# Optimization experiments

Measured on AMD Instinct MI355X. Metric: run time of the kernel, lower is better.

The kernel has to match this reference:

```python
import jax, jax.numpy as jnp
import numpy as np

B, N, CS = 4, 384, 384
CZ = 128
H, C, PQ, PV = 12, 16, 4, 8
INF, EPS = 1e5, 1e-8


def _rigid_apply(rot, trans, pts):
    # rot: [B,N,3,3], trans: [B,N,3], pts: [B,N,P,3]
    return jnp.einsum('bnij,bnpj->bnpi', rot, pts) + trans[:, :, None, :]


def _pts_from_linear(x, n_pts):
    # torch: split last dim into 3 chunks (x,y,z blocks) then stack on dim -1
    Bx, Nx = x.shape[:2]
    return jnp.moveaxis(x.reshape(Bx, Nx, 3, n_pts), -2, -1)  # [B,N,n_pts,3]


def _forward(s, z, rot, trans, mask, w_q, b_q, w_kv, b_kv, w_gq, b_gq, w_gk, b_gk,
             w_qp, b_qp, w_kvp, b_kvp, head_weights, w_out, b_out):
    del z  # z is an unused arg in the original forward
    Bx, Nx, _ = s.shape
    q = (s @ w_q + b_q).reshape(Bx, Nx, H, C)
    kv = (s @ w_kv + b_kv).reshape(Bx, Nx, H, 2 * C)
    k, v = kv[..., :C], kv[..., C:]
    # g_q / g_k are computed in the original but never used (dead code):
    _ = (s.sum(0) @ w_gq + b_gq)
    _ = (s.sum(0) @ w_gk + b_gk)

    q_pts = _pts_from_linear(s @ w_qp + b_qp, H * PQ)
    q_pts = _rigid_apply(rot, trans, q_pts).reshape(Bx, Nx, H, PQ, 3)
    kv_pts = _pts_from_linear(s @ w_kvp + b_kvp, H * (PQ + PV))
    kv_pts = _rigid_apply(rot, trans, kv_pts).reshape(Bx, Nx, H, PQ + PV, 3)
    k_pts, v_pts = kv_pts[..., :PQ, :], kv_pts[..., PQ:, :]

    scale = np.sqrt(1.0 / (3 * C)).astype(np.float32)
    a = jnp.einsum('bihc,bjhc->bhij', q, k) * scale  # [B,H,N,N]
    a_g = a  # original recomputes the identical q@k product

    # point-distance attention bias; diff is [B,N,N,H,PQ,3]
    diff = q_pts[:, :, None] - k_pts[:, None]
    sq = jnp.sum(diff * diff, axis=-1)  # [B,N,N,H,PQ]
    hw = jax.nn.softplus(head_weights) * np.sqrt(1.0 / (3 * (PQ * 9.0 / 2))).astype(np.float32)
    pt_att = -0.5 * jnp.sum(sq * hw[:, None], axis=-1)  # [B,N,N,H]
    pt_att = jnp.moveaxis(pt_att, -1, 1)  # [B,H,N,N]

    square_mask = INF * (mask[:, :, None] * mask[:, None, :] - 1.0)  # [B,N,N]
    a = jax.nn.softmax(a + square_mask[:, None] + a_g + pt_att, axis=-1)

    o = jnp.einsum('bhij,bjhc->bihc', a, v).reshape(Bx, Nx, H * C)
    o_pt = jnp.einsum('bhij,bjhpx->bihpx', a, v_pts)  # [B,N,H,PV,3]
    # invert_apply: rot^T (x - t)
    o_pt = jnp.einsum('bnji,bnhpj->bnhpi', rot, o_pt - trans[:, :, None, None, :])
    o_pt_norm = jnp.sqrt(jnp.sum(o_pt ** 2, axis=-1) + EPS).reshape(Bx, Nx, H * PV)
    o_pt = o_pt.reshape(Bx, Nx, H * PV, 3)
    cat = jnp.concatenate([o, o_pt[..., 0], o_pt[..., 1], o_pt[..., 2], o_pt_norm], axis=-1)
    return cat @ w_out + b_out


def setup_inputs() -> dict:
    key = jax.random.key(0)
    ks = jax.random.split(key, 16)
    lin = lambda k, fi, fo: jax.random.normal(k, (fi, fo), jnp.float32) / np.sqrt(fi).astype(np.float32)
    hc = H * C
    out_dim = H * (C + PV * 4)
    return {
        's': jax.random.normal(ks[0], (B, N, CS), jnp.float32),
        'z': jax.random.normal(ks[1], (B, N, N, CZ), jnp.float32),
        'rot': jnp.linalg.qr(jax.random.normal(ks[2], (B, N, 3, 3), jnp.float32))[0],
        'trans': jax.random.normal(ks[3], (B, N, 3), jnp.float32),
        'mask': jnp.ones((B, N), jnp.float32),
        'w_q': lin(ks[4], CS, hc), 'b_q': jnp.zeros((hc,), jnp.float32),
        'w_kv': lin(ks[5], CS, 2 * hc), 'b_kv': jnp.zeros((2 * hc,), jnp.float32),
        'w_gq': lin(ks[6], CS, hc), 'b_gq': jnp.zeros((hc,), jnp.float32),
        'w_gk': lin(ks[7], CS, hc), 'b_gk': jnp.zeros((hc,), jnp.float32),
        'w_qp': lin(ks[8], CS, H * PQ * 3), 'b_qp': jnp.zeros((H * PQ * 3,), jnp.float32),
        'w_kvp': lin(ks[9], CS, H * (PQ + PV) * 3), 'b_kvp': jnp.zeros((H * (PQ + PV) * 3,), jnp.float32),
        'head_weights': jnp.full((H,), 0.541324854, jnp.float32),  # softplus^-1(1)
        'w_out': lin(ks[10], out_dim, CS), 'b_out': jnp.zeros((CS,), jnp.float32),
    }


def reference(s, z, rot, trans, mask, w_q, b_q, w_kv, b_kv, w_gq, b_gq, w_gk, b_gk,
              w_qp, b_qp, w_kvp, b_kvp, head_weights, w_out, b_out):
    return _forward(s, z, rot, trans, mask, w_q, b_q, w_kv, b_kv, w_gq, b_gq, w_gk, b_gk,
                    w_qp, b_qp, w_kvp, b_kvp, head_weights, w_out, b_out)
```

## Files before the change

kernel.cpp:

```cpp
#include <hip/hip_runtime.h>
#include <math.h>

#define Bb 4
#define Nn 384
#define CSs 384
#define Hh 12
#define Cc 16
#define PQq 4
#define PVv 8
#define FPROJ 1152
#define FCAT 576
#define INFV 100000.0f
#define EPSV 1e-8f

#define WS_PROJ 0
#define WS_KP   1769472
#define WS_VP   2064384
#define WS_KPP  2359296
#define WS_VPP  2580480
#define WS_CAT  3022848
#define WS_QP   3907584
#define WS_QPP  4202496
#define WS_PART 4423680
#define PSTRIDE 2688
#define WS_WT   9068544
#define WS_WTO  9289728

typedef __attribute__((ext_vector_type(8))) short short8v;
typedef __attribute__((ext_vector_type(4))) float f32x4;

__device__ __forceinline__ short f2bf(float x) {
    unsigned u = __float_as_uint(x);
    unsigned r = (u + 0x7FFFu + ((u >> 16) & 1u)) >> 16;
    return (short)r;
}

__device__ __forceinline__ float get_bias(int f,
    const float* __restrict__ b_q, const float* __restrict__ b_kv,
    const float* __restrict__ b_qp, const float* __restrict__ b_kvp)
{
    if (f < 192) return b_q[f];
    if (f < 576) return b_kv[f - 192];
    if (f < 720) return b_qp[f - 576];
    return b_kvp[f - 720];
}

__global__ __launch_bounds__(256) void prep_kernel(
    const float* __restrict__ w_q, const float* __restrict__ w_kv,
    const float* __restrict__ w_qp, const float* __restrict__ w_kvp,
    const float* __restrict__ w_out,
    short* __restrict__ wt, short* __restrict__ wto)
{
    int idx = blockIdx.x * 256 + threadIdx.x;
    if (idx < 1152 * 384) {
        int f = idx / 384, k = idx % 384;
        float v;
        if (f < 192)      v = w_q[(size_t)k * 192 + f];
        else if (f < 576) v = w_kv[(size_t)k * 384 + (f - 192)];
        else if (f < 720) v = w_qp[(size_t)k * 144 + (f - 576)];
        else              v = w_kvp[(size_t)k * 432 + (f - 720)];
        wt[idx] = f2bf(v);
    } else if (idx < 1152 * 384 + 384 * 576) {
        int j = idx - 1152 * 384;
        int f = j / 576, k = j % 576;
        wto[j] = f2bf(w_out[(size_t)k * 384 + f]);
    }
}

__global__ __launch_bounds__(256) void proj_kernel(
    const float* __restrict__ s, const short* __restrict__ wt,
    const float* __restrict__ b_q, const float* __restrict__ b_kv,
    const float* __restrict__ b_qp, const float* __restrict__ b_kvp,
    float* __restrict__ proj)
{
    __shared__ short Al[64 * 40];
    __shared__ short Bl[64 * 40];

    const int bm = blockIdx.x % 24;
    const int bn = blockIdx.x / 24;
    const int m0 = bm * 64;
    const int f0 = bn * 64;
    const int t = threadIdx.x;
    const int w = t >> 6;
    const int lane = t & 63;
    const int lrow = lane & 15;
    const int lkg  = lane >> 4;

    const int srow = t >> 2;
    const int sseg = t & 3;

    f32x4 acc0 = {0,0,0,0}, acc1 = {0,0,0,0}, acc2 = {0,0,0,0}, acc3 = {0,0,0,0};

    for (int ks = 0; ks < 12; ++ks) {
        const int kbase = ks * 32;
        {
            const float* sp = s + (size_t)(m0 + srow) * CSs + kbase + sseg * 8;
            float4 v0 = *(const float4*)sp;
            float4 v1 = *(const float4*)(sp + 4);
            short8v a;
            a[0]=f2bf(v0.x); a[1]=f2bf(v0.y); a[2]=f2bf(v0.z); a[3]=f2bf(v0.w);
            a[4]=f2bf(v1.x); a[5]=f2bf(v1.y); a[6]=f2bf(v1.z); a[7]=f2bf(v1.w);
            *(short8v*)&Al[srow * 40 + sseg * 8] = a;
        }
        {
            short8v bvv = *(const short8v*)&wt[(size_t)(f0 + srow) * 384 + kbase + sseg * 8];
            *(short8v*)&Bl[srow * 40 + sseg * 8] = bvv;
        }
        __syncthreads();

        short8v av = *(const short8v*)&Al[(16 * w + lrow) * 40 + lkg * 8];
        short8v b0 = *(const short8v*)&Bl[(lrow) * 40 + lkg * 8];
        short8v b1 = *(const short8v*)&Bl[(16 + lrow) * 40 + lkg * 8];
        short8v b2 = *(const short8v*)&Bl[(32 + lrow) * 40 + lkg * 8];
        short8v b3 = *(const short8v*)&Bl[(48 + lrow) * 40 + lkg * 8];
        acc0 = __builtin_amdgcn_mfma_f32_16x16x32_bf16(av, b0, acc0, 0, 0, 0);
        acc1 = __builtin_amdgcn_mfma_f32_16x16x32_bf16(av, b1, acc1, 0, 0, 0);
        acc2 = __builtin_amdgcn_mfma_f32_16x16x32_bf16(av, b2, acc2, 0, 0, 0);
        acc3 = __builtin_amdgcn_mfma_f32_16x16x32_bf16(av, b3, acc3, 0, 0, 0);
        __syncthreads();
    }

    const int orow = m0 + 16 * w + lkg * 4;
#pragma unroll
    for (int e = 0; e < 4; ++e) {
        float* pr = proj + (size_t)(orow + e) * FPROJ + f0;
        int c0 = lrow;
        pr[c0]      = acc0[e] + get_bias(f0 + c0,      b_q, b_kv, b_qp, b_kvp);
        pr[16 + c0] = acc1[e] + get_bias(f0 + 16 + c0, b_q, b_kv, b_qp, b_kvp);
        pr[32 + c0] = acc2[e] + get_bias(f0 + 32 + c0, b_q, b_kv, b_qp, b_kvp);
        pr[48 + c0] = acc3[e] + get_bias(f0 + 48 + c0, b_q, b_kv, b_qp, b_kvp);
    }
}

__global__ __launch_bounds__(192) void pack_kernel(
    const float* __restrict__ proj,
    const float* __restrict__ rot, const float* __restrict__ trans,
    const float* __restrict__ hwts,
    float* __restrict__ Kp, float* __restrict__ Vp,
    float* __restrict__ KPp, float* __restrict__ VPp,
    float* __restrict__ Qp, float* __restrict__ QPp)
{
    const int bn = blockIdx.x;
    const int b = bn / Nn;
    const int n = bn % Nn;
    const int t = threadIdx.x;
    const float* R = rot + (size_t)bn * 9;
    const float* T = trans + (size_t)bn * 3;
    const float* pr = proj + (size_t)bn * FPROJ;

    if (t < 144) {
        float x = pr[720 + t];
        float y = pr[720 + 144 + t];
        float z = pr[720 + 288 + t];
        float ox = R[0]*x + R[1]*y + R[2]*z + T[0];
        float oy = R[3]*x + R[4]*y + R[5]*z + T[1];
        float oz = R[6]*x + R[7]*y + R[8]*z + T[2];
        int h = t / 12, pp = t % 12;
        int bh = b * Hh + h;
        if (pp < PQq) {
            float* o = KPp + ((size_t)(bh * Nn + n)) * 12 + pp * 3;
            o[0] = ox; o[1] = oy; o[2] = oz;
        } else {
            float* o = VPp + ((size_t)(bh * Nn + n)) * 24 + (pp - PQq) * 3;
            o[0] = ox; o[1] = oy; o[2] = oz;
        }
    }
    if (t < 48) {
        float x = pr[576 + t];
        float y = pr[576 + 48 + t];
        float z = pr[576 + 96 + t];
        float ox = R[0]*x + R[1]*y + R[2]*z + T[0];
        float oy = R[3]*x + R[4]*y + R[5]*z + T[1];
        float oz = R[6]*x + R[7]*y + R[8]*z + T[2];
        int h = t / 4, p = t % 4;
        float hw2 = log1pf(expf(hwts[h]));
        float n2wc = hw2 * 0.13608276348795434f;
        float* o = QPp + ((size_t)((b * Hh + h) * Nn + n)) * 12 + p * 3;
        o[0] = n2wc * ox; o[1] = n2wc * oy; o[2] = n2wc * oz;
    }
#pragma unroll
    for (int rep = 0; rep < 2; ++rep) {
        int idx = t + rep * 192;
        {
            int h = idx / 32, c2 = idx % 32;
            int bh = b * Hh + h;
            float v = pr[192 + h * 32 + c2];
            if (c2 < 16) Kp[((size_t)(bh * Nn + n)) * 16 + c2] = v;
            else         Vp[((size_t)(bh * Nn + n)) * 16 + (c2 - 16)] = v;
        }
        if (idx < 192) {
            int h = idx >> 4, c = idx & 15;
            int bh = b * Hh + h;
            Qp[((size_t)(bh * Nn + n)) * 16 + c] = 0.28867513459481287f * pr[idx];
        }
    }
}

__device__ __forceinline__ void store_hilo(short* H, short* L, int off, const float* vals) {
    short8v h0, h1, l0, l1;
#pragma unroll
    for (int k = 0; k < 8; ++k) {
        short hh = f2bf(vals[k]);
        float hf = __uint_as_float(((unsigned)(unsigned short)hh) << 16);
        h0[k] = hh; l0[k] = f2bf(vals[k] - hf);
    }
#pragma unroll
    for (int k = 0; k < 8; ++k) {
        short hh = f2bf(vals[k + 8]);
        float hf = __uint_as_float(((unsigned)(unsigned short)hh) << 16);
        h1[k] = hh; l1[k] = f2bf(vals[k + 8] - hf);
    }
    *(short8v*)&H[off]     = h0; *(short8v*)&H[off + 8] = h1;
    *(short8v*)&L[off]     = l0; *(short8v*)&L[off + 8] = l1;
}

__global__ __launch_bounds__(256) void attn_part_kernel(
    const float* __restrict__ Qp, const float* __restrict__ QPp,
    const float* __restrict__ Kp, const float* __restrict__ Vp,
    const float* __restrict__ KPp, const float* __restrict__ VPp,
    const float* __restrict__ mask, const float* __restrict__ hwts,
    float* __restrict__ part)
{
    __shared__ short smem_s[13696];
    short* Ahi = smem_s;
    short* Alo = smem_s + 2560;
    short* Khi = smem_s + 5120;
    short* Klo = smem_s + 7680;
    short* Vb  = smem_s + 10240;
    short* Pb  = smem_s;

    const int bid = blockIdx.x;
    const int jc = bid % 6;
    const int ic = (bid / 6) % 6;
    const int h  = (bid / 36) % Hh;
    const int b  = bid / (36 * Hh);
    const int t  = threadIdx.x;
    const int i0 = ic * 64;
    const int j0 = jc * 64;
    const int bh = b * Hh + h;

    const float hw = log1pf(expf(hwts[h]));
    const float wc = -0.5f * hw * 0.13608276348795434f;

    const float* QpB  = Qp  + ((size_t)(bh * Nn + i0)) * 16;
    const float* QPpB = QPp + ((size_t)(bh * Nn + i0)) * 12;
    const float* KpB  = Kp  + ((size_t)(bh * Nn + j0)) * 16;
    const float* VpB  = Vp  + ((size_t)(bh * Nn + j0)) * 16;
    const float* KPpB = KPp + ((size_t)(bh * Nn + j0)) * 12;
    const float* VPpB = VPp + ((size_t)(bh * Nn + j0)) * 24;
    const float* mb   = mask + b * Nn;

    if (t < 128) {
        const int i = t >> 1, half = t & 1;
        float vals[16];
        if (half == 0) {
            float4 a0 = *(const float4*)(QpB + i * 16);
            float4 a1 = *(const float4*)(QpB + i * 16 + 4);
            float4 a2 = *(const float4*)(QpB + i * 16 + 8);
            float4 a3 = *(const float4*)(QpB + i * 16 + 12);
            vals[0]=a0.x; vals[1]=a0.y; vals[2]=a0.z; vals[3]=a0.w;
            vals[4]=a1.x; vals[5]=a1.y; vals[6]=a1.z; vals[7]=a1.w;
            vals[8]=a2.x; vals[9]=a2.y; vals[10]=a2.z; vals[11]=a2.w;
            vals[12]=a3.x; vals[13]=a3.y; vals[14]=a3.z; vals[15]=a3.w;
        } else {
            float4 a0 = *(const float4*)(QPpB + i * 12);
            float4 a1 = *(const float4*)(QPpB + i * 12 + 4);
            float4 a2 = *(const float4*)(QPpB + i * 12 + 8);
            vals[0]=a0.x; vals[1]=a0.y; vals[2]=a0.z; vals[3]=a0.w;
            vals[4]=a1.x; vals[5]=a1.y; vals[6]=a1.z; vals[7]=a1.w;
            vals[8]=a2.x; vals[9]=a2.y; vals[10]=a2.z; vals[11]=a2.w;
            vals[12] = 1.0f;
            vals[13] = mb[i0 + i];
            vals[14] = 0.0f; vals[15] = 0.0f;
        }
        store_hilo(Ahi, Alo, i * 40 + half * 16, vals);
    } else {
        const int tt = t - 128, j = tt >> 1, half = tt & 1;
        float vals[16];
        if (half == 0) {
            float4 a0 = *(const float4*)(KpB + j * 16);
            float4 a1 = *(const float4*)(KpB + j * 16 + 4);
            float4 a2 = *(const float4*)(KpB + j * 16 + 8);
            float4 a3 = *(const float4*)(KpB + j * 16 + 12);
            vals[0]=a0.x; vals[1]=a0.y; vals[2]=a0.z; vals[3]=a0.w;
            vals[4]=a1.x; vals[5]=a1.y; vals[6]=a1.z; vals[7]=a1.w;
            vals[8]=a2.x; vals[9]=a2.y; vals[10]=a2.z; vals[11]=a2.w;
            vals[12]=a3.x; vals[13]=a3.y; vals[14]=a3.z; vals[15]=a3.w;
        } else {
            float4 a0 = *(const float4*)(KPpB + j * 12);
            float4 a1 = *(const float4*)(KPpB + j * 12 + 4);
            float4 a2 = *(const float4*)(KPpB + j * 12 + 8);
            vals[0]=a0.x; vals[1]=a0.y; vals[2]=a0.z; vals[3]=a0.w;
            vals[4]=a1.x; vals[5]=a1.y; vals[6]=a1.z; vals[7]=a1.w;
            vals[8]=a2.x; vals[9]=a2.y; vals[10]=a2.z; vals[11]=a2.w;
            float sq = a0.x*a0.x + a0.y*a0.y + a0.z*a0.z + a0.w*a0.w
                     + a1.x*a1.x + a1.y*a1.y + a1.z*a1.z + a1.w*a1.w
                     + a2.x*a2.x + a2.y*a2.y + a2.z*a2.z + a2.w*a2.w;
            vals[12] = wc * sq;
            vals[13] = INFV * (mb[j0 + j] - 1.0f);
            vals[14] = 0.0f; vals[15] = 0.0f;
        }
        store_hilo(Khi, Klo, j * 40 + half * 16, vals);
    }
    if (t < 128) {
        const int j = t >> 1, q = t & 1;
        float vv[20];
        if (q == 0) {
            float4 a0 = *(const float4*)(VpB + j * 16);
            float4 a1 = *(const float4*)(VpB + j * 16 + 4);
            float4 a2 = *(const float4*)(VpB + j * 16 + 8);
            float4 a3 = *(const float4*)(VpB + j * 16 + 12);
            float4 a4 = *(const float4*)(VPpB + j * 24);
            vv[0]=a0.x; vv[1]=a0.y; vv[2]=a0.z; vv[3]=a0.w;
            vv[4]=a1.x; vv[5]=a1.y; vv[6]=a1.z; vv[7]=a1.w;
            vv[8]=a2.x; vv[9]=a2.y; vv[10]=a2.z; vv[11]=a2.w;
            vv[12]=a3.x; vv[13]=a3.y; vv[14]=a3.z; vv[15]=a3.w;
            vv[16]=a4.x; vv[17]=a4.y; vv[18]=a4.z; vv[19]=a4.w;
        } else {
            float4 a0 = *(const float4*)(VPpB + j * 24 + 4);
            float4 a1 = *(const float4*)(VPpB + j * 24 + 8);
            float4 a2 = *(const float4*)(VPpB + j * 24 + 12);
            float4 a3 = *(const float4*)(VPpB + j * 24 + 16);
            float4 a4 = *(const float4*)(VPpB + j * 24 + 20);
            vv[0]=a0.x; vv[1]=a0.y; vv[2]=a0.z; vv[3]=a0.w;
            vv[4]=a1.x; vv[5]=a1.y; vv[6]=a1.z; vv[7]=a1.w;
            vv[8]=a2.x; vv[9]=a2.y; vv[10]=a2.z; vv[11]=a2.w;
            vv[12]=a3.x; vv[13]=a3.y; vv[14]=a3.z; vv[15]=a3.w;
            vv[16]=a4.x; vv[17]=a4.y; vv[18]=a4.z; vv[19]=a4.w;
        }
        const int c0 = q * 20;
#pragma unroll
        for (int k = 0; k < 20; ++k)
            Vb[(c0 + k) * 72 + j] = f2bf(vv[k]);
    } else {
        const int tt = t - 128;
        const int r = 40 + (tt >> 4);
        const int c0 = (tt & 15) * 4;
        Vb[r * 72 + c0 + 0] = 0; Vb[r * 72 + c0 + 1] = 0;
        Vb[r * 72 + c0 + 2] = 0; Vb[r * 72 + c0 + 3] = 0;
    }
    __syncthreads();

    const int w = t >> 6;
    const int lane = t & 63;
    const int lrow = lane & 15;
    const int lkg  = lane >> 4;

    f32x4 La0 = {0,0,0,0}, La1 = {0,0,0,0}, La2 = {0,0,0,0}, La3 = {0,0,0,0};
    {
        short8v ahi = *(const short8v*)&Ahi[(16 * w + lrow) * 40 + lkg * 8];
        short8v alo = *(const short8v*)&Alo[(16 * w + lrow) * 40 + lkg * 8];
        short8v k0h = *(const short8v*)&Khi[(lrow) * 40 + lkg * 8];
        short8v k1h = *(const short8v*)&Khi[(16 + lrow) * 40 + lkg * 8];
        short8v k2h = *(const short8v*)&Khi[(32 + lrow) * 40 + lkg * 8];
        short8v k3h = *(const short8v*)&Khi[(48 + lrow) * 40 + lkg * 8];
        short8v k0l = *(const short8v*)&Klo[(lrow) * 40 + lkg * 8];
        short8v k1l = *(const short8v*)&Klo[(16 + lrow) * 40 + lkg * 8];
        short8v k2l = *(const short8v*)&Klo[(32 + lrow) * 40 + lkg * 8];
        short8v k3l = *(const short8v*)&Klo[(48 + lrow) * 40 + lkg * 8];
        La0 = __builtin_amdgcn_mfma_f32_16x16x32_bf16(ahi, k0h, La0, 0, 0, 0);
        La1 = __builtin_amdgcn_mfma_f32_16x16x32_bf16(ahi, k1h, La1, 0, 0, 0);
        La2 = __builtin_amdgcn_mfma_f32_16x16x32_bf16(ahi, k2h, La2, 0, 0, 0);
        La3 = __builtin_amdgcn_mfma_f32_16x16x32_bf16(ahi, k3h, La3, 0, 0, 0);
        La0 = __builtin_amdgcn_mfma_f32_16x16x32_bf16(alo, k0h, La0, 0, 0, 0);
        La1 = __builtin_amdgcn_mfma_f32_16x16x32_bf16(alo, k1h, La1, 0, 0, 0);
        La2 = __builtin_amdgcn_mfma_f32_16x16x32_bf16(alo, k2h, La2, 0, 0, 0);
        La3 = __builtin_amdgcn_mfma_f32_16x16x32_bf16(alo, k3h, La3, 0, 0, 0);
        La0 = __builtin_amdgcn_mfma_f32_16x16x32_bf16(ahi, k0l, La0, 0, 0, 0);
        La1 = __builtin_amdgcn_mfma_f32_16x16x32_bf16(ahi, k1l, La1, 0, 0, 0);
        La2 = __builtin_amdgcn_mfma_f32_16x16x32_bf16(ahi, k2l, La2, 0, 0, 0);
        La3 = __builtin_amdgcn_mfma_f32_16x16x32_bf16(ahi, k3l, La3, 0, 0, 0);
    }

    const size_t pidx = ((size_t)(bh * 6 + ic)) * 6 + jc;
    float* po = part + pidx * PSTRIDE;

    float m0_, m1_, m2_, m3_, s0_, s1_, s2_, s3_;
    float p00,p10,p20,p30, p01,p11,p21,p31, p02,p12,p22,p32, p03,p13,p23,p33;

#define SMAX_E(E, TM, SM, P0, P1, P2, P3) { \
    float tmax_ = fmaxf(fmaxf(La0[E], La1[E]), fmaxf(La2[E], La3[E])); \
    tmax_ = fmaxf(tmax_, __shfl_xor(tmax_, 1)); \
    tmax_ = fmaxf(tmax_, __shfl_xor(tmax_, 2)); \
    tmax_ = fmaxf(tmax_, __shfl_xor(tmax_, 4)); \
    tmax_ = fmaxf(tmax_, __shfl_xor(tmax_, 8)); \
    P0 = __expf(La0[E] - tmax_); P1 = __expf(La1[E] - tmax_); \
    P2 = __expf(La2[E] - tmax_); P3 = __expf(La3[E] - tmax_); \
    float cs_ = P0 + P1 + P2 + P3; \
    cs_ += __shfl_xor(cs_, 1); cs_ += __shfl_xor(cs_, 2); \
    cs_ += __shfl_xor(cs_, 4); cs_ += __shfl_xor(cs_, 8); \
    TM = tmax_; SM = cs_; }

    SMAX_E(0, m0_, s0_, p00, p10, p20, p30);
    SMAX_E(1, m1_, s1_, p01, p11, p21, p31);
    SMAX_E(2, m2_, s2_, p02, p12, p22, p32);
    SMAX_E(3, m3_, s3_, p03, p13, p23, p33);
#undef SMAX_E

    if (lrow == 0) {
        int rb = 16 * w + 4 * lkg;
        po[2560 + rb + 0] = m0_; po[2624 + rb + 0] = s0_;
        po[2560 + rb + 1] = m1_; po[2624 + rb + 1] = s1_;
        po[2560 + rb + 2] = m2_; po[2624 + rb + 2] = s2_;
        po[2560 + rb + 3] = m3_; po[2624 + rb + 3] = s3_;
    }
    __syncthreads();

#define PW(E, PJ0, PJ1, PJ2, PJ3) { \
    int r_ = (16 * w + 4 * lkg + E) * 72; \
    Pb[r_ + lrow]      = f2bf(PJ0); \
    Pb[r_ + 16 + lrow] = f2bf(PJ1); \
    Pb[r_ + 32 + lrow] = f2bf(PJ2); \
    Pb[r_ + 48 + lrow] = f2bf(PJ3); }
    PW(0, p00, p10, p20, p30);
    PW(1, p01, p11, p21, p31);
    PW(2, p02, p12, p22, p32);
    PW(3, p03, p13, p23, p33);
#undef PW
    __syncthreads();

    f32x4 O0 = {0,0,0,0}, O1 = {0,0,0,0}, O2 = {0,0,0,0};
#pragma unroll
    for (int ch = 0; ch < 2; ++ch) {
        short8v pf = *(const short8v*)&Pb[(16 * w + lrow) * 72 + ch * 32 + lkg * 8];
        short8v v0 = *(const short8v*)&Vb[(lrow) * 72 + ch * 32 + lkg * 8];
        short8v v1 = *(const short8v*)&Vb[(16 + lrow) * 72 + ch * 32 + lkg * 8];
        short8v v2 = *(const short8v*)&Vb[(32 + lrow) * 72 + ch * 32 + lkg * 8];
        O0 = __builtin_amdgcn_mfma_f32_16x16x32_bf16(pf, v0, O0, 0, 0, 0);
        O1 = __builtin_amdgcn_mfma_f32_16x16x32_bf16(pf, v1, O1, 0, 0, 0);
        O2 = __builtin_amdgcn_mfma_f32_16x16x32_bf16(pf, v2, O2, 0, 0, 0);
    }
#pragma unroll
    for (int e = 0; e < 4; ++e) {
        int r = 16 * w + 4 * lkg + e;
        po[r * 40 + lrow]      = O0[e];
        po[r * 40 + 16 + lrow] = O1[e];
        if (lrow < 8) po[r * 40 + 32 + lrow] = O2[e];
    }
}

__global__ __launch_bounds__(256) void attn_merge_kernel(
    const float* __restrict__ part,
    const float* __restrict__ rot, const float* __restrict__ trans,
    float* __restrict__ cat)
{
    __shared__ float wsh[64 * 8];
    __shared__ float ob[64 * 44];

    const int bid = blockIdx.x;
    const int ic = bid % 6;
    const int h  = (bid / 6) % Hh;
    const int b  = bid / (6 * Hh);
    const int t  = threadIdx.x;
    const int i0 = ic * 64;
    const int bh = b * Hh + h;
    const size_t pbase = (((size_t)(bh * 6 + ic)) * 6) * PSTRIDE;

    if (t < 64) {
        float mk[6], sk[6];
        float M = -3.0e38f;
#pragma unroll
        for (int k = 0; k < 6; ++k) {
            mk[k] = part[pbase + (size_t)k * PSTRIDE + 2560 + t];
            sk[k] = part[pbase + (size_t)k * PSTRIDE + 2624 + t];
            M = fmaxf(M, mk[k]);
        }
        float wk[6]; float stot = 0.0f;
#pragma unroll
        for (int k = 0; k < 6; ++k) {
            wk[k] = __expf(mk[k] - M);
            stot += wk[k] * sk[k];
        }
        float inv = 1.0f / stot;
#pragma unroll
        for (int k = 0; k < 6; ++k) wsh[t * 8 + k] = wk[k] * inv;
    }
    __syncthreads();

#pragma unroll
    for (int it = 0; it < 10; ++it) {
        int idx = t + it * 256;
        int row = idx / 40, col = idx % 40;
        float v = 0.0f;
#pragma unroll
        for (int k = 0; k < 6; ++k)
            v += wsh[row * 8 + k] * part[pbase + (size_t)k * PSTRIDE + row * 40 + col];
        ob[row * 44 + col] = v;
    }
    __syncthreads();

    {
        const int i = t >> 2;
        const int qq = t & 3;
        const int bnI = b * Nn + i0 + i;
        float* crow = cat + (size_t)bnI * FCAT;

        float4 o = *(const float4*)&ob[i * 44 + 4 * qq];
        *(float4*)&crow[h * 16 + 4 * qq] = o;

        const float* R = rot + (size_t)bnI * 9;
        const float* T = trans + (size_t)bnI * 3;
#pragma unroll
        for (int e = 0; e < 2; ++e) {
            int pe = qq + 4 * e;
            float g0 = ob[i * 44 + 16 + 3 * pe + 0] - T[0];
            float g1 = ob[i * 44 + 16 + 3 * pe + 1] - T[1];
            float g2 = ob[i * 44 + 16 + 3 * pe + 2] - T[2];
            float lx = R[0]*g0 + R[3]*g1 + R[6]*g2;
            float ly = R[1]*g0 + R[4]*g1 + R[7]*g2;
            float lz = R[2]*g0 + R[5]*g1 + R[8]*g2;
            crow[192 + h * 8 + pe] = lx;
            crow[288 + h * 8 + pe] = ly;
            crow[384 + h * 8 + pe] = lz;
            crow[480 + h * 8 + pe] = sqrtf(lx*lx + ly*ly + lz*lz + EPSV);
        }
    }
}

__global__ __launch_bounds__(256) void out_kernel(
    const float* __restrict__ cat, const short* __restrict__ wto,
    const float* __restrict__ b_out, float* __restrict__ out)
{
    __shared__ short Al[64 * 40];
    __shared__ short Bl[64 * 40];

    const int bm = blockIdx.x % 24;
    const int bn = blockIdx.x / 24;
    const int m0 = bm * 64;
    const int n0 = bn * 64;
    const int t = threadIdx.x;
    const int w = t >> 6;
    const int lane = t & 63;
    const int lrow = lane & 15;
    const int lkg  = lane >> 4;

    const int srow = t >> 2;
    const int sseg = t & 3;

    f32x4 acc0 = {0,0,0,0}, acc1 = {0,0,0,0}, acc2 = {0,0,0,0}, acc3 = {0,0,0,0};

    for (int ks = 0; ks < 18; ++ks) {
        const int kbase = ks * 32;
        {
            const float* cp = cat + (size_t)(m0 + srow) * FCAT + kbase + sseg * 8;
            float4 v0 = *(const float4*)cp;
            float4 v1 = *(const float4*)(cp + 4);
            short8v a;
            a[0]=f2bf(v0.x); a[1]=f2bf(v0.y); a[2]=f2bf(v0.z); a[3]=f2bf(v0.w);
            a[4]=f2bf(v1.x); a[5]=f2bf(v1.y); a[6]=f2bf(v1.z); a[7]=f2bf(v1.w);
            *(short8v*)&Al[srow * 40 + sseg * 8] = a;
        }
        {
            short8v bvv = *(const short8v*)&wto[(size_t)(n0 + srow) * FCAT + kbase + sseg * 8];
            *(short8v*)&Bl[srow * 40 + sseg * 8] = bvv;
        }
        __syncthreads();

        short8v av = *(const short8v*)&Al[(16 * w + lrow) * 40 + lkg * 8];
        short8v b0 = *(const short8v*)&Bl[(lrow) * 40 + lkg * 8];
        short8v b1 = *(const short8v*)&Bl[(16 + lrow) * 40 + lkg * 8];
        short8v b2 = *(const short8v*)&Bl[(32 + lrow) * 40 + lkg * 8];
        short8v b3 = *(const short8v*)&Bl[(48 + lrow) * 40 + lkg * 8];
        acc0 = __builtin_amdgcn_mfma_f32_16x16x32_bf16(av, b0, acc0, 0, 0, 0);
        acc1 = __builtin_amdgcn_mfma_f32_16x16x32_bf16(av, b1, acc1, 0, 0, 0);
        acc2 = __builtin_amdgcn_mfma_f32_16x16x32_bf16(av, b2, acc2, 0, 0, 0);
        acc3 = __builtin_amdgcn_mfma_f32_16x16x32_bf16(av, b3, acc3, 0, 0, 0);
        __syncthreads();
    }

    const int orow = m0 + 16 * w + lkg * 4;
#pragma unroll
    for (int e = 0; e < 4; ++e) {
        float* pr = out + (size_t)(orow + e) * 384 + n0;
        int c0 = lrow;
        pr[c0]      = acc0[e] + b_out[n0 + c0];
        pr[16 + c0] = acc1[e] + b_out[n0 + 16 + c0];
        pr[32 + c0] = acc2[e] + b_out[n0 + 32 + c0];
        pr[48 + c0] = acc3[e] + b_out[n0 + 48 + c0];
    }
}

extern "C" void kernel_launch(void* const* d_in, const int* in_sizes, int n_in,
                              void* d_out, int out_size, void* d_ws, size_t ws_size,
                              hipStream_t stream) {
    const float* s     = (const float*)d_in[0];
    const float* rot   = (const float*)d_in[2];
    const float* trans = (const float*)d_in[3];
    const float* mask  = (const float*)d_in[4];
    const float* w_q   = (const float*)d_in[5];
    const float* b_q   = (const float*)d_in[6];
    const float* w_kv  = (const float*)d_in[7];
    const float* b_kv  = (const float*)d_in[8];
    const float* w_qp  = (const float*)d_in[13];
    const float* b_qp  = (const float*)d_in[14];
    const float* w_kvp = (const float*)d_in[15];
    const float* b_kvp = (const float*)d_in[16];
    const float* hwts  = (const float*)d_in[17];
    const float* w_out = (const float*)d_in[18];
    const float* b_out = (const float*)d_in[19];

    float* ws    = (float*)d_ws;
    float* proj  = ws + WS_PROJ;
    float* Kp    = ws + WS_KP;
    float* Vp    = ws + WS_VP;
    float* KPp   = ws + WS_KPP;
    float* VPp   = ws + WS_VPP;
    float* catb  = ws + WS_CAT;
    float* Qp    = ws + WS_QP;
    float* QPp   = ws + WS_QPP;
    float* partb = ws + WS_PART;
    short* wt    = (short*)(ws + WS_WT);
    short* wto   = (short*)(ws + WS_WTO);
    float* out   = (float*)d_out;

    hipLaunchKernelGGL(prep_kernel, dim3(2592), dim3(256), 0, stream,
                       w_q, w_kv, w_qp, w_kvp, w_out, wt, wto);
    hipLaunchKernelGGL(proj_kernel, dim3(432), dim3(256), 0, stream,
                       s, wt, b_q, b_kv, b_qp, b_kvp, proj);
    hipLaunchKernelGGL(pack_kernel, dim3(1536), dim3(192), 0, stream,
                       proj, rot, trans, hwts, Kp, Vp, KPp, VPp, Qp, QPp);
    hipLaunchKernelGGL(attn_part_kernel, dim3(1728), dim3(256), 0, stream,
                       Qp, QPp, Kp, Vp, KPp, VPp, mask, hwts, partb);
    hipLaunchKernelGGL(attn_merge_kernel, dim3(288), dim3(256), 0, stream,
                       partb, rot, trans, catb);
    hipLaunchKernelGGL(out_kernel, dim3(144), dim3(256), 0, stream,
                       catb, wto, b_out, out);
}
```

Before: 60.20 us.

## Pre-pack bf16 hi/lo attention operands in pack kernel and store concat as bf16

The pack kernel now builds the augmented Q/K rows (scaled q, weighted points, mask and squared-norm columns) and the V rows, splits them into bf16 hi/lo pairs, and writes them in the layout the attention kernel stages into shared memory. The attention kernel then copies bf16 vectors instead of redoing the conversion and norm work in each of its 36 tiles per head. The merge kernel also writes the concatenated features as bf16, which halves the traffic read by the output GEMM. In exchange the pack kernel does more work and uses shared memory, and the workspace gains new buffers.

```diff
diff --git a/kernel.cpp b/kernel.cpp
--- a/kernel.cpp
+++ b/kernel.cpp
@@ -14,17 +14,16 @@
 #define EPSV 1e-8f
 
 #define WS_PROJ 0
-#define WS_KP   1769472
-#define WS_VP   2064384
-#define WS_KPP  2359296
-#define WS_VPP  2580480
 #define WS_CAT  3022848
-#define WS_QP   3907584
-#define WS_QPP  4202496
 #define WS_PART 4423680
 #define PSTRIDE 2688
 #define WS_WT   9068544
 #define WS_WTO  9289728
+#define WS_AH   9400320
+#define WS_AL   9695232
+#define WS_KH   9990144
+#define WS_KL   10285056
+#define WS_VBP  10579968
 
 typedef __attribute__((ext_vector_type(8))) short short8v;
 typedef __attribute__((ext_vector_type(4))) float f32x4;
@@ -33,6 +32,9 @@
     unsigned u = __float_as_uint(x);
     unsigned r = (u + 0x7FFFu + ((u >> 16) & 1u)) >> 16;
     return (short)r;
+}
+__device__ __forceinline__ float bf2f(short h) {
+    return __uint_as_float(((unsigned)(unsigned short)h) << 16);
 }
 
 __device__ __forceinline__ float get_bias(int f,
@@ -135,11 +137,16 @@
 __global__ __launch_bounds__(192) void pack_kernel(
     const float* __restrict__ proj,
     const float* __restrict__ rot, const float* __restrict__ trans,
-    const float* __restrict__ hwts,
-    float* __restrict__ Kp, float* __restrict__ Vp,
-    float* __restrict__ KPp, float* __restrict__ VPp,
-    float* __restrict__ Qp, float* __restrict__ QPp)
-{
+    const float* __restrict__ hwts, const float* __restrict__ mask,
+    short* __restrict__ Ah, short* __restrict__ Al,
+    short* __restrict__ Kh, short* __restrict__ Kl,
+    short* __restrict__ Vbp)
+{
+    __shared__ float abuf[12 * 32];
+    __shared__ float kbuf[12 * 32];
+    __shared__ float vbuf[12 * 40];
+    __shared__ float kpsq[12 * 4];
+
     const int bn = blockIdx.x;
     const int b = bn / Nn;
     const int n = bn % Nn;
@@ -147,6 +154,7 @@
     const float* R = rot + (size_t)bn * 9;
     const float* T = trans + (size_t)bn * 3;
     const float* pr = proj + (size_t)bn * FPROJ;
+    const float mi = mask[bn];
 
     if (t < 144) {
         float x = pr[720 + t];
@@ -156,13 +164,15 @@
         float oy = R[3]*x + R[4]*y + R[5]*z + T[1];
         float oz = R[6]*x + R[7]*y + R[8]*z + T[2];
         int h = t / 12, pp = t % 12;
-        int bh = b * Hh + h;
         if (pp < PQq) {
-            float* o = KPp + ((size_t)(bh * Nn + n)) * 12 + pp * 3;
-            o[0] = ox; o[1] = oy; o[2] = oz;
+            kbuf[h*32 + 16 + pp*3 + 0] = ox;
+            kbuf[h*32 + 16 + pp*3 + 1] = oy;
+            kbuf[h*32 + 16 + pp*3 + 2] = oz;
+            kpsq[h*4 + pp] = ox*ox + oy*oy + oz*oz;
         } else {
-            float* o = VPp + ((size_t)(bh * Nn + n)) * 24 + (pp - PQq) * 3;
-            o[0] = ox; o[1] = oy; o[2] = oz;
+            vbuf[h*40 + 16 + (pp - PQq)*3 + 0] = ox;
+            vbuf[h*40 + 16 + (pp - PQq)*3 + 1] = oy;
+            vbuf[h*40 + 16 + (pp - PQq)*3 + 2] = oz;
         }
     }
     if (t < 48) {
@@ -173,52 +183,69 @@
         float oy = R[3]*x + R[4]*y + R[5]*z + T[1];
         float oz = R[6]*x + R[7]*y + R[8]*z + T[2];
         int h = t / 4, p = t % 4;
-        float hw2 = log1pf(expf(hwts[h]));
-        float n2wc = hw2 * 0.13608276348795434f;
-        float* o = QPp + ((size_t)((b * Hh + h) * Nn + n)) * 12 + p * 3;
-        o[0] = n2wc * ox; o[1] = n2wc * oy; o[2] = n2wc * oz;
-    }
-#pragma unroll
-    for (int rep = 0; rep < 2; ++rep) {
-        int idx = t + rep * 192;
-        {
-            int h = idx / 32, c2 = idx % 32;
-            int bh = b * Hh + h;
-            float v = pr[192 + h * 32 + c2];
-            if (c2 < 16) Kp[((size_t)(bh * Nn + n)) * 16 + c2] = v;
-            else         Vp[((size_t)(bh * Nn + n)) * 16 + (c2 - 16)] = v;
-        }
-        if (idx < 192) {
-            int h = idx >> 4, c = idx & 15;
-            int bh = b * Hh + h;
-            Qp[((size_t)(bh * Nn + n)) * 16 + c] = 0.28867513459481287f * pr[idx];
-        }
-    }
-}
-
-__device__ __forceinline__ void store_hilo(short* H, short* L, int off, const float* vals) {
-    short8v h0, h1, l0, l1;
-#pragma unroll
-    for (int k = 0; k < 8; ++k) {
-        short hh = f2bf(vals[k]);
-        float hf = __uint_as_float(((unsigned)(unsigned short)hh) << 16);
-        h0[k] = hh; l0[k] = f2bf(vals[k] - hf);
-    }
-#pragma unroll
-    for (int k = 0; k < 8; ++k) {
-        short hh = f2bf(vals[k + 8]);
-        float hf = __uint_as_float(((unsigned)(unsigned short)hh) << 16);
-        h1[k] = hh; l1[k] = f2bf(vals[k + 8] - hf);
-    }
-    *(short8v*)&H[off]     = h0; *(short8v*)&H[off + 8] = h1;
-    *(short8v*)&L[off]     = l0; *(short8v*)&L[off + 8] = l1;
+        float n2wc = log1pf(expf(hwts[h])) * 0.13608276348795434f;
+        abuf[h*32 + 16 + p*3 + 0] = n2wc * ox;
+        abuf[h*32 + 16 + p*3 + 1] = n2wc * oy;
+        abuf[h*32 + 16 + p*3 + 2] = n2wc * oz;
+    }
+    {
+        int h = t >> 4, c = t & 15;
+        abuf[h*32 + c] = 0.28867513459481287f * pr[h * 16 + c];
+        kbuf[h*32 + c] = pr[192 + h * 32 + c];
+        vbuf[h*40 + c] = pr[192 + h * 32 + 16 + c];
+    }
+    if (t < 12) {
+        abuf[t*32 + 28] = 1.0f;  abuf[t*32 + 29] = mi;
+        abuf[t*32 + 30] = 0.0f;  abuf[t*32 + 31] = 0.0f;
+        kbuf[t*32 + 29] = INFV * (mi - 1.0f);
+        kbuf[t*32 + 30] = 0.0f;  kbuf[t*32 + 31] = 0.0f;
+    }
+    __syncthreads();
+    if (t < 12) {
+        float hw2 = log1pf(expf(hwts[t]));
+        float wc = -0.5f * hw2 * 0.13608276348795434f;
+        kbuf[t*32 + 28] = wc * (kpsq[t*4] + kpsq[t*4+1] + kpsq[t*4+2] + kpsq[t*4+3]);
+    }
+    __syncthreads();
+
+    if (t < 48) {
+        int h = t >> 2, pc = t & 3;
+        const float* src = &abuf[h*32 + pc*8];
+        short8v hi, lo;
+#pragma unroll
+        for (int k = 0; k < 8; ++k) {
+            short hh = f2bf(src[k]);
+            hi[k] = hh; lo[k] = f2bf(src[k] - bf2f(hh));
+        }
+        size_t off = ((size_t)((b * Hh + h) * Nn + n)) * 32 + pc * 8;
+        *(short8v*)&Ah[off] = hi;
+        *(short8v*)&Al[off] = lo;
+    } else if (t < 96) {
+        int tt = t - 48, h = tt >> 2, pc = tt & 3;
+        const float* src = &kbuf[h*32 + pc*8];
+        short8v hi, lo;
+#pragma unroll
+        for (int k = 0; k < 8; ++k) {
+            short hh = f2bf(src[k]);
+            hi[k] = hh; lo[k] = f2bf(src[k] - bf2f(hh));
+        }
+        size_t off = ((size_t)((b * Hh + h) * Nn + n)) * 32 + pc * 8;
+        *(short8v*)&Kh[off] = hi;
+        *(short8v*)&Kl[off] = lo;
+    } else if (t < 156) {
+        int tt = t - 96, h = tt / 5, pc = tt % 5;
+        const float* src = &vbuf[h*40 + pc*8];
+        short8v v;
+#pragma unroll
+        for (int k = 0; k < 8; ++k) v[k] = f2bf(src[k]);
+        *(short8v*)&Vbp[((size_t)((b * Hh + h) * Nn + n)) * 40 + pc * 8] = v;
+    }
 }
 
 __global__ __launch_bounds__(256) void attn_part_kernel(
-    const float* __restrict__ Qp, const float* __restrict__ QPp,
-    const float* __restrict__ Kp, const float* __restrict__ Vp,
-    const float* __restrict__ KPp, const float* __restrict__ VPp,
-    const float* __restrict__ mask, const float* __restrict__ hwts,
+    const short* __restrict__ Ah, const short* __restrict__ Al,
+    const short* __restrict__ Kh, const short* __restrict__ Kl,
+    const short* __restrict__ Vbp,
     float* __restrict__ part)
 {
     __shared__ short smem_s[13696];
@@ -239,105 +266,29 @@
     const int j0 = jc * 64;
     const int bh = b * Hh + h;
 
-    const float hw = log1pf(expf(hwts[h]));
-    const float wc = -0.5f * hw * 0.13608276348795434f;
-
-    const float* QpB  = Qp  + ((size_t)(bh * Nn + i0)) * 16;
-    const float* QPpB = QPp + ((size_t)(bh * Nn + i0)) * 12;
-    const float* KpB  = Kp  + ((size_t)(bh * Nn + j0)) * 16;
-    const float* VpB  = Vp  + ((size_t)(bh * Nn + j0)) * 16;
-    const float* KPpB = KPp + ((size_t)(bh * Nn + j0)) * 12;
-    const float* VPpB = VPp + ((size_t)(bh * Nn + j0)) * 24;
-    const float* mb   = mask + b * Nn;
-
-    if (t < 128) {
-        const int i = t >> 1, half = t & 1;
-        float vals[16];
-        if (half == 0) {
-            float4 a0 = *(const float4*)(QpB + i * 16);
-            float4 a1 = *(const float4*)(QpB + i * 16 + 4);
-            float4 a2 = *(const float4*)(QpB + i * 16 + 8);
-            float4 a3 = *(const float4*)(QpB + i * 16 + 12);
-            vals[0]=a0.x; vals[1]=a0.y; vals[2]=a0.z; vals[3]=a0.w;
-            vals[4]=a1.x; vals[5]=a1.y; vals[6]=a1.z; vals[7]=a1.w;
-            vals[8]=a2.x; vals[9]=a2.y; vals[10]=a2.z; vals[11]=a2.w;
-            vals[12]=a3.x; vals[13]=a3.y; vals[14]=a3.z; vals[15]=a3.w;
-        } else {
-            float4 a0 = *(const float4*)(QPpB + i * 12);
-            float4 a1 = *(const float4*)(QPpB + i * 12 + 4);
-            float4 a2 = *(const float4*)(QPpB + i * 12 + 8);
-            vals[0]=a0.x; vals[1]=a0.y; vals[2]=a0.z; vals[3]=a0.w;
-            vals[4]=a1.x; vals[5]=a1.y; vals[6]=a1.z; vals[7]=a1.w;
-            vals[8]=a2.x; vals[9]=a2.y; vals[10]=a2.z; vals[11]=a2.w;
-            vals[12] = 1.0f;
-            vals[13] = mb[i0 + i];
-            vals[14] = 0.0f; vals[15] = 0.0f;
-        }
-        store_hilo(Ahi, Alo, i * 40 + half * 16, vals);
-    } else {
-        const int tt = t - 128, j = tt >> 1, half = tt & 1;
-        float vals[16];
-        if (half == 0) {
-            float4 a0 = *(const float4*)(KpB + j * 16);
-            float4 a1 = *(const float4*)(KpB + j * 16 + 4);
-            float4 a2 = *(const float4*)(KpB + j * 16 + 8);
-            float4 a3 = *(const float4*)(KpB + j * 16 + 12);
-            vals[0]=a0.x; vals[1]=a0.y; vals[2]=a0.z; vals[3]=a0.w;
-            vals[4]=a1.x; vals[5]=a1.y; vals[6]=a1.z; vals[7]=a1.w;
-            vals[8]=a2.x; vals[9]=a2.y; vals[10]=a2.z; vals[11]=a2.w;
-            vals[12]=a3.x; vals[13]=a3.y; vals[14]=a3.z; vals[15]=a3.w;
-        } else {
-            float4 a0 = *(const float4*)(KPpB + j * 12);
-            float4 a1 = *(const float4*)(KPpB + j * 12 + 4);
-            float4 a2 = *(const float4*)(KPpB + j * 12 + 8);
-            vals[0]=a0.x; vals[1]=a0.y; vals[2]=a0.z; vals[3]=a0.w;
-            vals[4]=a1.x; vals[5]=a1.y; vals[6]=a1.z; vals[7]=a1.w;
-            vals[8]=a2.x; vals[9]=a2.y; vals[10]=a2.z; vals[11]=a2.w;
-            float sq = a0.x*a0.x + a0.y*a0.y + a0.z*a0.z + a0.w*a0.w
-                     + a1.x*a1.x + a1.y*a1.y + a1.z*a1.z + a1.w*a1.w
-                     + a2.x*a2.x + a2.y*a2.y + a2.z*a2.z + a2.w*a2.w;
-            vals[12] = wc * sq;
-            vals[13] = INFV * (mb[j0 + j] - 1.0f);
-            vals[14] = 0.0f; vals[15] = 0.0f;
-        }
-        store_hilo(Khi, Klo, j * 40 + half * 16, vals);
-    }
-    if (t < 128) {
-        const int j = t >> 1, q = t & 1;
-        float vv[20];
-        if (q == 0) {
-            float4 a0 = *(const float4*)(VpB + j * 16);
-            float4 a1 = *(const float4*)(VpB + j * 16 + 4);
-            float4 a2 = *(const float4*)(VpB + j * 16 + 8);
-            float4 a3 = *(const float4*)(VpB + j * 16 + 12);
-            float4 a4 = *(const float4*)(VPpB + j * 24);
-            vv[0]=a0.x; vv[1]=a0.y; vv[2]=a0.z; vv[3]=a0.w;
-            vv[4]=a1.x; vv[5]=a1.y; vv[6]=a1.z; vv[7]=a1.w;
-            vv[8]=a2.x; vv[9]=a2.y; vv[10]=a2.z; vv[11]=a2.w;
-            vv[12]=a3.x; vv[13]=a3.y; vv[14]=a3.z; vv[15]=a3.w;
-            vv[16]=a4.x; vv[17]=a4.y; vv[18]=a4.z; vv[19]=a4.w;
-        } else {
-            float4 a0 = *(const float4*)(VPpB + j * 24 + 4);
-            float4 a1 = *(const float4*)(VPpB + j * 24 + 8);
-            float4 a2 = *(const float4*)(VPpB + j * 24 + 12);
-            float4 a3 = *(const float4*)(VPpB + j * 24 + 16);
-            float4 a4 = *(const float4*)(VPpB + j * 24 + 20);
-            vv[0]=a0.x; vv[1]=a0.y; vv[2]=a0.z; vv[3]=a0.w;
-            vv[4]=a1.x; vv[5]=a1.y; vv[6]=a1.z; vv[7]=a1.w;
-            vv[8]=a2.x; vv[9]=a2.y; vv[10]=a2.z; vv[11]=a2.w;
-            vv[12]=a3.x; vv[13]=a3.y; vv[14]=a3.z; vv[15]=a3.w;
-            vv[16]=a4.x; vv[17]=a4.y; vv[18]=a4.z; vv[19]=a4.w;
-        }
-        const int c0 = q * 20;
-#pragma unroll
-        for (int k = 0; k < 20; ++k)
-            Vb[(c0 + k) * 72 + j] = f2bf(vv[k]);
-    } else {
-        const int tt = t - 128;
-        const int r = 40 + (tt >> 4);
-        const int c0 = (tt & 15) * 4;
-        Vb[r * 72 + c0 + 0] = 0; Vb[r * 72 + c0 + 1] = 0;
-        Vb[r * 72 + c0 + 2] = 0; Vb[r * 72 + c0 + 3] = 0;
+    const short* AhB = Ah + ((size_t)(bh * Nn + i0)) * 32;
+    const short* AlB = Al + ((size_t)(bh * Nn + i0)) * 32;
+    const short* KhB = Kh + ((size_t)(bh * Nn + j0)) * 32;
+    const short* KlB = Kl + ((size_t)(bh * Nn + j0)) * 32;
+    const short* VbB = Vbp + ((size_t)(bh * Nn + j0)) * 40;
+
+    {
+        const int i = t >> 2, pc = t & 3;
+        *(short8v*)&Ahi[i * 40 + pc * 8] = *(const short8v*)&AhB[i * 32 + pc * 8];
+        *(short8v*)&Alo[i * 40 + pc * 8] = *(const short8v*)&AlB[i * 32 + pc * 8];
+        *(short8v*)&Khi[i * 40 + pc * 8] = *(const short8v*)&KhB[i * 32 + pc * 8];
+        *(short8v*)&Klo[i * 40 + pc * 8] = *(const short8v*)&KlB[i * 32 + pc * 8];
+    }
+#pragma unroll
+    for (int e = t; e < 320; e += 256) {
+        int j = e / 5, pc = e % 5;
+        short8v v = *(const short8v*)&VbB[j * 40 + pc * 8];
+#pragma unroll
+        for (int k = 0; k < 8; ++k) Vb[(pc * 8 + k) * 72 + j] = v[k];
+    }
+    if (t < 144) {
+        int o = 40 * 72 + t * 4;
+        Vb[o] = 0; Vb[o+1] = 0; Vb[o+2] = 0; Vb[o+3] = 0;
     }
     __syncthreads();
 
@@ -442,7 +393,7 @@
 __global__ __launch_bounds__(256) void attn_merge_kernel(
     const float* __restrict__ part,
     const float* __restrict__ rot, const float* __restrict__ trans,
-    float* __restrict__ cat)
+    short* __restrict__ cat_bf)
 {
     __shared__ float wsh[64 * 8];
     __shared__ float ob[64 * 44];
@@ -493,10 +444,13 @@
         const int i = t >> 2;
         const int qq = t & 3;
         const int bnI = b * Nn + i0 + i;
-        float* crow = cat + (size_t)bnI * FCAT;
+        short* crow = cat_bf + (size_t)bnI * FCAT;
 
         float4 o = *(const float4*)&ob[i * 44 + 4 * qq];
-        *(float4*)&crow[h * 16 + 4 * qq] = o;
+        crow[h * 16 + 4 * qq + 0] = f2bf(o.x);
+        crow[h * 16 + 4 * qq + 1] = f2bf(o.y);
+        crow[h * 16 + 4 * qq + 2] = f2bf(o.z);
+        crow[h * 16 + 4 * qq + 3] = f2bf(o.w);
 
         const float* R = rot + (size_t)bnI * 9;
         const float* T = trans + (size_t)bnI * 3;
@@ -509,16 +463,16 @@
             float lx = R[0]*g0 + R[3]*g1 + R[6]*g2;
             float ly = R[1]*g0 + R[4]*g1 + R[7]*g2;
             float lz = R[2]*g0 + R[5]*g1 + R[8]*g2;
-            crow[192 + h * 8 + pe] = lx;
-            crow[288 + h * 8 + pe] = ly;
-            crow[384 + h * 8 + pe] = lz;
-            crow[480 + h * 8 + pe] = sqrtf(lx*lx + ly*ly + lz*lz + EPSV);
+            crow[192 + h * 8 + pe] = f2bf(lx);
+            crow[288 + h * 8 + pe] = f2bf(ly);
+            crow[384 + h * 8 + pe] = f2bf(lz);
+            crow[480 + h * 8 + pe] = f2bf(sqrtf(lx*lx + ly*ly + lz*lz + EPSV));
         }
     }
 }
 
 __global__ __launch_bounds__(256) void out_kernel(
-    const float* __restrict__ cat, const short* __restrict__ wto,
+    const short* __restrict__ cat_bf, const short* __restrict__ wto,
     const float* __restrict__ b_out, float* __restrict__ out)
 {
     __shared__ short Al[64 * 40];
@@ -542,12 +496,7 @@
     for (int ks = 0; ks < 18; ++ks) {
         const int kbase = ks * 32;
         {
-            const float* cp = cat + (size_t)(m0 + srow) * FCAT + kbase + sseg * 8;
-            float4 v0 = *(const float4*)cp;
-            float4 v1 = *(const float4*)(cp + 4);
-            short8v a;
-            a[0]=f2bf(v0.x); a[1]=f2bf(v0.y); a[2]=f2bf(v0.z); a[3]=f2bf(v0.w);
-            a[4]=f2bf(v1.x); a[5]=f2bf(v1.y); a[6]=f2bf(v1.z); a[7]=f2bf(v1.w);
+            short8v a = *(const short8v*)&cat_bf[(size_t)(m0 + srow) * FCAT + kbase + sseg * 8];
             *(short8v*)&Al[srow * 40 + sseg * 8] = a;
         }
         {
@@ -601,16 +550,15 @@
 
     float* ws    = (float*)d_ws;
     float* proj  = ws + WS_PROJ;
-    float* Kp    = ws + WS_KP;
-    float* Vp    = ws + WS_VP;
-    float* KPp   = ws + WS_KPP;
-    float* VPp   = ws + WS_VPP;
-    float* catb  = ws + WS_CAT;
-    float* Qp    = ws + WS_QP;
-    float* QPp   = ws + WS_QPP;
+    short* cat_bf = (short*)(ws + WS_CAT);
     float* partb = ws + WS_PART;
     short* wt    = (short*)(ws + WS_WT);
     short* wto   = (short*)(ws + WS_WTO);
+    short* Ah    = (short*)(ws + WS_AH);
+    short* Alp   = (short*)(ws + WS_AL);
+    short* Kh    = (short*)(ws + WS_KH);
+    short* Kl    = (short*)(ws + WS_KL);
+    short* Vbp   = (short*)(ws + WS_VBP);
     float* out   = (float*)d_out;
 
     hipLaunchKernelGGL(prep_kernel, dim3(2592), dim3(256), 0, stream,
@@ -618,11 +566,11 @@
     hipLaunchKernelGGL(proj_kernel, dim3(432), dim3(256), 0, stream,
                        s, wt, b_q, b_kv, b_qp, b_kvp, proj);
     hipLaunchKernelGGL(pack_kernel, dim3(1536), dim3(192), 0, stream,
-                       proj, rot, trans, hwts, Kp, Vp, KPp, VPp, Qp, QPp);
+                       proj, rot, trans, hwts, mask, Ah, Alp, Kh, Kl, Vbp);
     hipLaunchKernelGGL(attn_part_kernel, dim3(1728), dim3(256), 0, stream,
-                       Qp, QPp, Kp, Vp, KPp, VPp, mask, hwts, partb);
+                       Ah, Alp, Kh, Kl, Vbp, partb);
     hipLaunchKernelGGL(attn_merge_kernel, dim3(288), dim3(256), 0, stream,
-                       partb, rot, trans, catb);
+                       partb, rot, trans, cat_bf);
     hipLaunchKernelGGL(out_kernel, dim3(144), dim3(256), 0, stream,
-                       catb, wto, b_out, out);
-}
+                       cat_bf, wto, b_out, out);
+}
```

Result: faster. 55.46 us (-7.9%).
